# Kernel tuning notes

Measured on AMD Instinct MI355X. Metric: run time of the kernel, lower is better.

The kernel has to match this reference:

```python
import jax, jax.numpy as jnp
import numpy as np

N = 100000      # nodes
E = 3200000     # edges
F_IN = 128      # input node features
G = 64          # graphs in batch
A = 32          # action_shape


def _fanin_uniform(key, shape):
    v = 1.0 / np.sqrt(shape[0])
    return jax.random.uniform(key, shape, jnp.float32, -v, v)


def setup_inputs() -> dict:
    key = jax.random.key(0)
    ks = jax.random.split(key, 16)
    x = jax.random.normal(ks[0], (N, F_IN), jnp.float32)
    edge_index = jax.random.randint(ks[1], (2, E), 0, N, jnp.int64)
    batch = jnp.sort(jax.random.randint(ks[2], (N,), 0, G, jnp.int64))
    init_w = 0.003
    return {
        "x": x,
        "edge_index": edge_index,
        "batch": batch,
        # GCN weights are [in, out] (old-style PyG GCNConv .weight)
        "W1": _fanin_uniform(ks[3], (F_IN, 16)), "b1": jnp.zeros((16,), jnp.float32),
        "W2": _fanin_uniform(ks[4], (16, 64)),   "b2": jnp.zeros((64,), jnp.float32),
        "W3": _fanin_uniform(ks[5], (64, 32)),   "b3": jnp.zeros((32,), jnp.float32),
        # MLP head (Linear stores [out, in]; we keep [in, out] and matmul directly)
        "Wa": _fanin_uniform(ks[6], (32, 64)),   "ba": jnp.zeros((64,), jnp.float32),
        "Wo": jax.random.uniform(ks[7], (64, A), jnp.float32, -init_w, init_w),
        "bo": jnp.zeros((A,), jnp.float32),
    }


def _gcn_conv(x, W, b, src, dst, dinv):
    # GCNConv: D^{-1/2}(A+I)D^{-1/2} X W + b, symmetric norm with self-loops.
    h = x @ W                                   # [N, out] small GEMM
    coef = dinv[src] * dinv[dst]                # [E]
    msg = h[src] * coef[:, None]                # gather + scale (memory-bound)
    agg = jax.ops.segment_sum(msg, dst, num_segments=N)  # scatter-add
    agg = agg + h * (dinv * dinv)[:, None]      # self-loop contribution
    return agg + b


def reference(x, edge_index, batch, W1, b1, W2, b2, W3, b3, Wa, ba, Wo, bo):
    src, dst = edge_index[0], edge_index[1]
    # degree with self-loops (edge weights = 1)
    deg = jax.ops.segment_sum(jnp.ones((E,), x.dtype), dst, num_segments=N) + 1.0
    dinv = jax.lax.rsqrt(deg)

    h = jax.nn.relu(_gcn_conv(x, W1, b1, src, dst, dinv))   # dropout: eval no-op
    h = jax.nn.relu(_gcn_conv(h, W2, b2, src, dst, dinv))
    h = _gcn_conv(h, W3, b3, src, dst, dinv)                # [N, 32]

    # global_mean_pool over batch ids
    sums = jax.ops.segment_sum(h, batch, num_segments=G)            # [G, 32]
    cnts = jax.ops.segment_sum(jnp.ones((N,), h.dtype), batch, num_segments=G)
    pooled = sums / jnp.maximum(cnts, 1.0)[:, None]

    a = jax.nn.relu(pooled @ Wa + ba)
    return jnp.tanh(a @ Wo + bo)                             # [G, A]
```

## Files before the change

kernel.cpp:

```cpp
#include <hip/hip_runtime.h>
#include <hip/hip_bf16.h>
#include <math.h>


#define THREADS 256
#define TCSR 512
#define BSH 8
#define MAXNB 512
#define CH_E 2048
#define CPT 8

__device__ inline unsigned short f2bf(float f) {
    unsigned int u = __float_as_uint(f);
    return (unsigned short)((u + 0x7fffu + ((u >> 16) & 1u)) >> 16);
}
__device__ inline unsigned int pk2bf(float a, float b) {
    return (unsigned int)f2bf(a) | ((unsigned int)f2bf(b) << 16);
}
__device__ inline float bflo(unsigned int u) { return __uint_as_float(u << 16); }
__device__ inline float bfhi(unsigned int u) { return __uint_as_float(u & 0xffff0000u); }
__device__ inline void unpk8(const uint4 u, float* f) {
    f[0] = bflo(u.x); f[1] = bfhi(u.x); f[2] = bflo(u.y); f[3] = bfhi(u.y);
    f[4] = bflo(u.z); f[5] = bfhi(u.z); f[6] = bflo(u.w); f[7] = bfhi(u.w);
}

__global__ void k_countA(const int* __restrict__ dst, unsigned short* __restrict__ lp16,
                         int* __restrict__ cnt_mat, int E, int NB, int NCH) {
    __shared__ int hist[MAXNB];
    int t = threadIdx.x, chunk = blockIdx.x;
    for (int h = t; h < NB; h += THREADS) hist[h] = 0;
    __syncthreads();
    int e0 = chunk * CH_E, e1 = min(E, e0 + CH_E);
    for (int e = e0 + t; e < e1; e += THREADS) {
        int h = dst[e] >> BSH;
        int lp = atomicAdd(&hist[h], 1);
        lp16[e] = (unsigned short)lp;
    }
    __syncthreads();
    for (int h = t; h < NB; h += THREADS) cnt_mat[(size_t)h * NCH + chunk] = hist[h];
}

__global__ void k_sumK1(const int* __restrict__ cnt_mat, int* __restrict__ bucket_tot, int NCH) {
    __shared__ int red[THREADS];
    int b = blockIdx.x, t = threadIdx.x;
    int s = 0;
    for (int c = t; c < NCH; c += THREADS) s += cnt_mat[(size_t)b * NCH + c];
    red[t] = s;
    __syncthreads();
    for (int off = THREADS / 2; off > 0; off >>= 1) {
        if (t < off) red[t] += red[t + off];
        __syncthreads();
    }
    if (t == 0) bucket_tot[b] = red[0];
}

__global__ void k_scanK2(const int* __restrict__ bucket_tot, int* __restrict__ bucket_base,
                         int* __restrict__ rowptr, int NB, int E, int N) {
    __shared__ int sh[MAXNB];
    int t = threadIdx.x;
    int v = (t < NB) ? bucket_tot[t] : 0;
    sh[t] = v;
    __syncthreads();
    for (int off = 1; off < MAXNB; off <<= 1) {
        int u = (t >= off) ? sh[t - off] : 0;
        __syncthreads();
        sh[t] += u;
        __syncthreads();
    }
    if (t < NB) bucket_base[t] = sh[t] - v;
    if (t == 0) { bucket_base[NB] = E; rowptr[N] = E; }
}

__global__ void k_scanK3(const int* __restrict__ cnt_mat, const int* __restrict__ bucket_base,
                         int* __restrict__ offs_mat, int NCH) {
    __shared__ int sh[THREADS];
    int b = blockIdx.x, t = threadIdx.x;
    int c0 = t * CPT;
    int v[CPT];
    int s = 0;
#pragma unroll
    for (int k = 0; k < CPT; ++k) {
        int c = c0 + k;
        v[k] = (c < NCH) ? cnt_mat[(size_t)b * NCH + c] : 0;
        s += v[k];
    }
    sh[t] = s;
    __syncthreads();
    for (int off = 1; off < THREADS; off <<= 1) {
        int u = (t >= off) ? sh[t - off] : 0;
        __syncthreads();
        sh[t] += u;
        __syncthreads();
    }
    int run = bucket_base[b] + sh[t] - s;
#pragma unroll
    for (int k = 0; k < CPT; ++k) {
        int c = c0 + k;
        if (c < NCH) { offs_mat[(size_t)b * NCH + c] = run; run += v[k]; }
    }
}

__global__ void k_scatter2(const int* __restrict__ src, const int* __restrict__ dst,
                           const unsigned short* __restrict__ lp16,
                           const int* __restrict__ offs_mat,
                           unsigned int* __restrict__ bedges, int E, int NB, int NCH) {
    __shared__ int offs[MAXNB];
    int t = threadIdx.x, chunk = blockIdx.x;
    for (int h = t; h < NB; h += THREADS) offs[h] = offs_mat[(size_t)h * NCH + chunk];
    __syncthreads();
    int e0 = chunk * CH_E, e1 = min(E, e0 + CH_E);
    for (int e = e0 + t; e < e1; e += THREADS) {
        int d = dst[e];
        int h = d >> BSH;
        int pos = offs[h] + (int)lp16[e];
        bedges[pos] = ((unsigned int)src[e] << BSH) | (unsigned int)(d & ((1 << BSH) - 1));
    }
}

__global__ void k_bucket_csr(const unsigned int* __restrict__ bedges,
                             const int* __restrict__ bucket_base,
                             int* __restrict__ rowptr, float* __restrict__ dinv,
                             int* __restrict__ csr_src, int N) {
    __shared__ int hist[256];
    __shared__ int sc[256];
    __shared__ int cur[256];
    int t = threadIdx.x;
    int b = blockIdx.x;
    int base = bucket_base[b];
    int end = bucket_base[b + 1];
    if (t < 256) hist[t] = 0;
    __syncthreads();
    for (int i = base + t; i < end; i += TCSR)
        atomicAdd(&hist[bedges[i] & 255], 1);
    __syncthreads();
    int c = 0;
    if (t < 256) { c = hist[t]; sc[t] = c; }
    __syncthreads();
    for (int off = 1; off < 256; off <<= 1) {
        int u = (t >= off && t < 256) ? sc[t - off] : 0;
        __syncthreads();
        if (t < 256) sc[t] += u;
        __syncthreads();
    }
    if (t < 256) {
        int excl = sc[t] - c;
        int node = (b << BSH) + t;
        if (node < N) {
            rowptr[node] = base + excl;
            dinv[node] = (float)(1.0 / sqrt((double)(c + 1)));
        }
        cur[t] = excl;
    }
    __syncthreads();
    for (int i = base + t; i < end; i += TCSR) {
        unsigned int u = bedges[i];
        int ln = (int)(u & 255);
        int p = atomicAdd(&cur[ln], 1);
        csr_src[base + p] = (int)(u >> BSH);
    }
}

__global__ __launch_bounds__(256) void k_gemm1(const float* __restrict__ X,
                        const float* __restrict__ W,
                        const float* __restrict__ dinv, unsigned short* __restrict__ H, int N) {
    __shared__ float Wt[16 * 128];
    int t = threadIdx.x;
    for (int i = t; i < 16 * 128; i += THREADS) {
        int j = i >> 7, k = i & 127;
        Wt[i] = W[k * 16 + j];
    }
    __syncthreads();
    int row = blockIdx.x * THREADS + t;
    if (row >= N) return;
    const float4* xr = (const float4*)(X + (size_t)row * 128);
    float acc[16];
#pragma unroll
    for (int j = 0; j < 16; ++j) acc[j] = 0.0f;
#pragma unroll 4
    for (int k4 = 0; k4 < 32; ++k4) {
        float4 xv = xr[k4];
#pragma unroll
        for (int j = 0; j < 16; ++j) {
            const float4 wv = *(const float4*)&Wt[j * 128 + k4 * 4];
            acc[j] += xv.x * wv.x + xv.y * wv.y + xv.z * wv.z + xv.w * wv.w;
        }
    }
    float di = dinv[row];
    uint4 oa, ob;
    oa.x = pk2bf(acc[0] * di, acc[1] * di);
    oa.y = pk2bf(acc[2] * di, acc[3] * di);
    oa.z = pk2bf(acc[4] * di, acc[5] * di);
    oa.w = pk2bf(acc[6] * di, acc[7] * di);
    ob.x = pk2bf(acc[8] * di, acc[9] * di);
    ob.y = pk2bf(acc[10] * di, acc[11] * di);
    ob.z = pk2bf(acc[12] * di, acc[13] * di);
    ob.w = pk2bf(acc[14] * di, acc[15] * di);
    uint4* outr = (uint4*)(H + (size_t)row * 16);
    outr[0] = oa;
    outr[1] = ob;
}

template<int F, int MODE, int S>
__global__ __launch_bounds__(256) void k_pull(
        const int* __restrict__ rowptr, const int* __restrict__ csr_src,
        const float* __restrict__ dinv, const unsigned short* __restrict__ Hb,
        const float* __restrict__ bias, void* __restrict__ outp,
        const int* __restrict__ batch, float* __restrict__ gsums,
        int N, int G) {
    const int LPN = F / 8;
    const int GRP = LPN * S;
    const int NPB = THREADS / GRP;
    int t = threadIdx.x;
    int idx = t % GRP;
    int fl = idx % LPN;
    int s  = idx / LPN;
    int fo = fl * 8;
    int node = blockIdx.x * NPB + t / GRP;

    float acc[8] = {0.f, 0.f, 0.f, 0.f, 0.f, 0.f, 0.f, 0.f};
    if (node < N) {
        int beg = rowptr[node], end = rowptr[node + 1];
        int i = beg + s;
        for (; i + 3 * S < end; i += 4 * S) {
            int s0 = csr_src[i];
            int s1 = csr_src[i + S];
            int s2 = csr_src[i + 2 * S];
            int s3 = csr_src[i + 3 * S];
            uint4 g0 = *(const uint4*)(Hb + (size_t)s0 * F + fo);
            uint4 g1 = *(const uint4*)(Hb + (size_t)s1 * F + fo);
            uint4 g2 = *(const uint4*)(Hb + (size_t)s2 * F + fo);
            uint4 g3 = *(const uint4*)(Hb + (size_t)s3 * F + fo);
            float f0[8], f1[8], f2[8], f3[8];
            unpk8(g0, f0); unpk8(g1, f1); unpk8(g2, f2); unpk8(g3, f3);
#pragma unroll
            for (int j = 0; j < 8; ++j) acc[j] += (f0[j] + f1[j]) + (f2[j] + f3[j]);
        }
        for (; i < end; i += S) {
            int sv = csr_src[i];
            uint4 g = *(const uint4*)(Hb + (size_t)sv * F + fo);
            float f[8];
            unpk8(g, f);
#pragma unroll
            for (int j = 0; j < 8; ++j) acc[j] += f[j];
        }
    }
#pragma unroll
    for (int j = 0; j < 8; ++j) {
        if (S >= 2) acc[j] += __shfl_xor(acc[j], LPN);
        if (S >= 4) acc[j] += __shfl_xor(acc[j], 2 * LPN);
    }

    if constexpr (MODE == 3) {
        __shared__ float lsum[4][32];
        __shared__ int g0s;
        for (int z = t; z < 4 * 32; z += THREADS) ((float*)lsum)[z] = 0.0f;
        if (t == 0) g0s = batch[blockIdx.x * NPB];
        __syncthreads();
        int g0 = g0s;
        if (node < N && s == 0) {
            uint4 gs = *(const uint4*)(Hb + (size_t)node * F + fo);
            float sf[8];
            unpk8(gs, sf);
            float di = dinv[node];
            int g = batch[node];
            int r = g - g0;
            if ((unsigned)r < 4u) {
#pragma unroll
                for (int j = 0; j < 8; ++j)
                    atomicAdd(&lsum[r][fo + j], di * (acc[j] + sf[j]));
            } else {
#pragma unroll
                for (int j = 0; j < 8; ++j)
                    atomicAdd(&gsums[(size_t)g * 32 + fo + j], di * (acc[j] + sf[j]));
            }
        }
        __syncthreads();
        if (t < 128) {
            int r = t >> 5, f = t & 31;
            int g = g0 + r;
            float v = lsum[r][f];
            if (g < G && v != 0.0f) atomicAdd(&gsums[(size_t)g * 32 + f], v);
        }
    } else {
        if (node < N && s == 0) {
            uint4 gs = *(const uint4*)(Hb + (size_t)node * F + fo);
            float sf[8];
            unpk8(gs, sf);
            float di = dinv[node];
            float tv[8];
#pragma unroll
            for (int j = 0; j < 8; ++j) tv[j] = di * (acc[j] + sf[j]);
            if constexpr (MODE == 1) {
                float w[8];
#pragma unroll
                for (int j = 0; j < 8; ++j) w[j] = fmaxf(tv[j] + bias[fo + j], 0.0f) * di;
                uint4 st;
                st.x = pk2bf(w[0], w[1]); st.y = pk2bf(w[2], w[3]);
                st.z = pk2bf(w[4], w[5]); st.w = pk2bf(w[6], w[7]);
                *(uint4*)((unsigned short*)outp + (size_t)node * F + fo) = st;
            } else {
                float* of = (float*)outp + (size_t)node * F + fo;
                float4 o0, o1;
                o0.x = tv[0]; o0.y = tv[1]; o0.z = tv[2]; o0.w = tv[3];
                o1.x = tv[4]; o1.y = tv[5]; o1.z = tv[6]; o1.w = tv[7];
                ((float4*)of)[0] = o0; ((float4*)of)[1] = o1;
            }
        }
    }
}

__global__ __launch_bounds__(256) void k_mlp(const float* __restrict__ P2,
                      const float* __restrict__ W2, const float* __restrict__ b2,
                      const float* __restrict__ W3, const float* __restrict__ dinv,
                      unsigned short* __restrict__ Hb3, int N) {
    __shared__ float W2t[64][16];
    __shared__ float W3t[32][64];
    __shared__ float b2s[64];
    int t = threadIdx.x;
    for (int i = t; i < 64 * 16; i += THREADS) W2t[i / 16][i % 16] = W2[(i % 16) * 64 + (i / 16)];
    for (int i = t; i < 32 * 64; i += THREADS) W3t[i / 64][i % 64] = W3[(i % 64) * 32 + (i / 64)];
    if (t < 64) b2s[t] = b2[t];
    __syncthreads();
    int n = blockIdx.x * THREADS + t;
    if (n >= N) return;
    const float4* pr = (const float4*)(P2 + (size_t)n * 16);
    float4 p0 = pr[0], p1 = pr[1], p2v = pr[2], p3 = pr[3];
    float p[16] = { p0.x, p0.y, p0.z, p0.w, p1.x, p1.y, p1.z, p1.w,
                    p2v.x, p2v.y, p2v.z, p2v.w, p3.x, p3.y, p3.z, p3.w };
    float a[64];
#pragma unroll
    for (int j = 0; j < 64; ++j) {
        const float4* w = (const float4*)W2t[j];
        float4 w0 = w[0], w1 = w[1], w2q = w[2], w3q = w[3];
        float acc = b2s[j];
        acc += p[0] * w0.x + p[1] * w0.y + p[2] * w0.z + p[3] * w0.w;
        acc += p[4] * w1.x + p[5] * w1.y + p[6] * w1.z + p[7] * w1.w;
        acc += p[8] * w2q.x + p[9] * w2q.y + p[10] * w2q.z + p[11] * w2q.w;
        acc += p[12] * w3q.x + p[13] * w3q.y + p[14] * w3q.z + p[15] * w3q.w;
        a[j] = fmaxf(acc, 0.0f);
    }
    float di = dinv[n];
    unsigned short* outr = Hb3 + (size_t)n * 32;
#pragma unroll
    for (int m = 0; m < 32; m += 2) {
        float o0 = 0.0f, o1 = 0.0f;
        const float4* wa = (const float4*)W3t[m];
        const float4* wb = (const float4*)W3t[m + 1];
#pragma unroll
        for (int q = 0; q < 16; ++q) {
            float4 va = wa[q], vb = wb[q];
            o0 += a[4 * q] * va.x + a[4 * q + 1] * va.y + a[4 * q + 2] * va.z + a[4 * q + 3] * va.w;
            o1 += a[4 * q] * vb.x + a[4 * q + 1] * vb.y + a[4 * q + 2] * vb.z + a[4 * q + 3] * vb.w;
        }
        *(unsigned int*)(outr + m) = pk2bf(o0 * di, o1 * di);
    }
}

__global__ void k_zero_f(float* p, int n) {
    int i = blockIdx.x * blockDim.x + threadIdx.x;
    if (i < n) p[i] = 0.0f;
}

__global__ void k_head(const float* __restrict__ sums, const int* __restrict__ batch, int N,
                       const float* __restrict__ b3,
                       const float* __restrict__ Wa, const float* __restrict__ ba,
                       const float* __restrict__ Wo, const float* __restrict__ bo,
                       float* __restrict__ out) {
    int g = blockIdx.x;
    int j = threadIdx.x;
    int lo = 0, hi = N;
    while (lo < hi) { int m = (lo + hi) >> 1; if (batch[m] < g) lo = m + 1; else hi = m; }
    int start = lo;
    lo = start; hi = N;
    while (lo < hi) { int m = (lo + hi) >> 1; if (batch[m] < g + 1) lo = m + 1; else hi = m; }
    int cnt = lo - start;
    float inv = 1.0f / (float)(cnt > 0 ? cnt : 1);

    __shared__ float p[32];
    __shared__ float a[64];
    if (j < 32) p[j] = sums[g * 32 + j] * inv + b3[j];
    __syncthreads();
    float acc = ba[j];
#pragma unroll
    for (int k = 0; k < 32; ++k) acc += p[k] * Wa[k * 64 + j];
    a[j] = fmaxf(acc, 0.0f);
    __syncthreads();
    if (j < 32) {
        float acc2 = bo[j];
#pragma unroll
        for (int k = 0; k < 64; ++k) acc2 += a[k] * Wo[k * 32 + j];
        out[g * 32 + j] = tanhf(acc2);
    }
}

static inline int cdiv(long long a, int b) { return (int)((a + b - 1) / b); }
static inline size_t align256(size_t x) { return (x + 255) & ~(size_t)255; }

extern "C" void kernel_launch(void* const* d_in, const int* in_sizes, int n_in,
                              void* d_out, int out_size, void* d_ws, size_t ws_size,
                              hipStream_t stream) {
    const float* x     = (const float*)d_in[0];
    const int*   edge  = (const int*)d_in[1];
    const int*   batch = (const int*)d_in[2];
    const float* W1 = (const float*)d_in[3];  const float* b1 = (const float*)d_in[4];
    const float* W2 = (const float*)d_in[5];  const float* b2 = (const float*)d_in[6];
    const float* W3 = (const float*)d_in[7];  const float* b3 = (const float*)d_in[8];
    const float* Wa = (const float*)d_in[9];  const float* ba = (const float*)d_in[10];
    const float* Wo = (const float*)d_in[11]; const float* bo = (const float*)d_in[12];

    const int E = in_sizes[1] / 2;
    const int N = in_sizes[2];
    const int G = 64;
    const int NB = cdiv(N, 1 << BSH);
    const int NCH = cdiv(E, CH_E);

    const int* srcp = edge;
    const int* dstp = edge + E;

    char* base = (char*)d_ws;
    size_t off = 0;
    float* dinv   = (float*)(base + off); off = align256(off + sizeof(float) * N);
    unsigned short* lp16 = (unsigned short*)(base + off); off = align256(off + sizeof(short) * E);
    int* cnt_mat  = (int*)(base + off); off = align256(off + sizeof(int) * (size_t)NB * NCH);
    int* offs_mat = (int*)(base + off); off = align256(off + sizeof(int) * (size_t)NB * NCH);
    int* btot     = (int*)(base + off); off = align256(off + sizeof(int) * (NB + 1));
    int* bbase    = (int*)(base + off); off = align256(off + sizeof(int) * (NB + 1));
    unsigned int* bedges = (unsigned int*)(base + off); off = align256(off + sizeof(int) * E);
    int* rowptr   = (int*)(base + off); off = align256(off + sizeof(int) * (N + 1));
    int* csr_src  = (int*)(base + off); off = align256(off + sizeof(int) * E);
    unsigned short* Hb1 = (unsigned short*)(base + off); off = align256(off + sizeof(short) * (size_t)N * 16);
    unsigned short* Hb2 = (unsigned short*)(base + off); off = align256(off + sizeof(short) * (size_t)N * 16);
    float* P2     = (float*)(base + off); off = align256(off + sizeof(float) * (size_t)N * 16);
    unsigned short* Hb3 = (unsigned short*)(base + off); off = align256(off + sizeof(short) * (size_t)N * 32);
    float* sums   = (float*)(base + off); off = align256(off + sizeof(float) * G * 32);

    k_countA<<<NCH, THREADS, 0, stream>>>(dstp, lp16, cnt_mat, E, NB, NCH);
    k_sumK1<<<NB, THREADS, 0, stream>>>(cnt_mat, btot, NCH);
    k_scanK2<<<1, MAXNB, 0, stream>>>(btot, bbase, rowptr, NB, E, N);
    k_scanK3<<<NB, THREADS, 0, stream>>>(cnt_mat, bbase, offs_mat, NCH);
    k_scatter2<<<NCH, THREADS, 0, stream>>>(srcp, dstp, lp16, offs_mat, bedges, E, NB, NCH);

    k_bucket_csr<<<NB, TCSR, 0, stream>>>(bedges, bbase, rowptr, dinv, csr_src, N);

    k_gemm1<<<cdiv(N, THREADS), THREADS, 0, stream>>>(x, W1, dinv, Hb1, N);
    k_pull<16, 1, 4><<<cdiv(N, 32), THREADS, 0, stream>>>(rowptr, csr_src, dinv, Hb1, b1, Hb2,
                                                          nullptr, nullptr, N, G);

    k_pull<16, 2, 4><<<cdiv(N, 32), THREADS, 0, stream>>>(rowptr, csr_src, dinv, Hb2, nullptr, P2,
                                                          nullptr, nullptr, N, G);

    k_mlp<<<cdiv(N, THREADS), THREADS, 0, stream>>>(P2, W2, b2, W3, dinv, Hb3, N);

    k_zero_f<<<cdiv(G * 32, THREADS), THREADS, 0, stream>>>(sums, G * 32);
    k_pull<32, 3, 2><<<cdiv(N, 32), THREADS, 0, stream>>>(rowptr, csr_src, dinv, Hb3, nullptr,
                                                          nullptr, batch, sums, N, G);

    k_head<<<G, 64, 0, stream>>>(sums, batch, N, b3, Wa, ba, Wo, bo, (float*)d_out);
}
```

Measured before the change: 339.4 us.

## Split per-node MLP across 8 threads with shared-memory hidden activations

The fused per-node MLP (16->64 relu ->32) used to run one node per thread, holding 64 hidden activations in registers. Now 8 threads cooperate on each pair of nodes: each computes a slice of the hidden layer, stages it in padded shared memory, then computes a slice of the outputs. This cuts register pressure and spreads the work over more threads to raise occupancy and parallelism. In exchange it adds a block barrier, extra shared memory traffic and strided 2-byte output stores instead of packed 4-byte stores.

```diff
diff --git a/kernel.cpp b/kernel.cpp
--- a/kernel.cpp
+++ b/kernel.cpp
@@ -313,46 +313,84 @@
                       const float* __restrict__ W2, const float* __restrict__ b2,
                       const float* __restrict__ W3, const float* __restrict__ dinv,
                       unsigned short* __restrict__ Hb3, int N) {
-    __shared__ float W2t[64][16];
-    __shared__ float W3t[32][64];
+    __shared__ float W2p[64 * 20];
+    __shared__ float W3p[32 * 68];
     __shared__ float b2s[64];
+    __shared__ float a_sh[64 * 72];
     int t = threadIdx.x;
-    for (int i = t; i < 64 * 16; i += THREADS) W2t[i / 16][i % 16] = W2[(i % 16) * 64 + (i / 16)];
-    for (int i = t; i < 32 * 64; i += THREADS) W3t[i / 64][i % 64] = W3[(i % 64) * 32 + (i / 64)];
+    for (int i = t; i < 64 * 16; i += THREADS) {
+        int j = i >> 4, k = i & 15;
+        W2p[j * 20 + k] = W2[k * 64 + j];
+    }
+    for (int i = t; i < 32 * 64; i += THREADS) {
+        int m = i >> 6, k = i & 63;
+        W3p[m * 68 + k] = W3[k * 32 + m];
+    }
     if (t < 64) b2s[t] = b2[t];
     __syncthreads();
-    int n = blockIdx.x * THREADS + t;
-    if (n >= N) return;
-    const float4* pr = (const float4*)(P2 + (size_t)n * 16);
-    float4 p0 = pr[0], p1 = pr[1], p2v = pr[2], p3 = pr[3];
-    float p[16] = { p0.x, p0.y, p0.z, p0.w, p1.x, p1.y, p1.z, p1.w,
-                    p2v.x, p2v.y, p2v.z, p2v.w, p3.x, p3.y, p3.z, p3.w };
-    float a[64];
-#pragma unroll
-    for (int j = 0; j < 64; ++j) {
-        const float4* w = (const float4*)W2t[j];
-        float4 w0 = w[0], w1 = w[1], w2q = w[2], w3q = w[3];
-        float acc = b2s[j];
-        acc += p[0] * w0.x + p[1] * w0.y + p[2] * w0.z + p[3] * w0.w;
-        acc += p[4] * w1.x + p[5] * w1.y + p[6] * w1.z + p[7] * w1.w;
-        acc += p[8] * w2q.x + p[9] * w2q.y + p[10] * w2q.z + p[11] * w2q.w;
-        acc += p[12] * w3q.x + p[13] * w3q.y + p[14] * w3q.z + p[15] * w3q.w;
-        a[j] = fmaxf(acc, 0.0f);
-    }
-    float di = dinv[n];
-    unsigned short* outr = Hb3 + (size_t)n * 32;
-#pragma unroll
-    for (int m = 0; m < 32; m += 2) {
-        float o0 = 0.0f, o1 = 0.0f;
-        const float4* wa = (const float4*)W3t[m];
-        const float4* wb = (const float4*)W3t[m + 1];
-#pragma unroll
-        for (int q = 0; q < 16; ++q) {
-            float4 va = wa[q], vb = wb[q];
-            o0 += a[4 * q] * va.x + a[4 * q + 1] * va.y + a[4 * q + 2] * va.z + a[4 * q + 3] * va.w;
-            o1 += a[4 * q] * vb.x + a[4 * q + 1] * vb.y + a[4 * q + 2] * vb.z + a[4 * q + 3] * vb.w;
-        }
-        *(unsigned int*)(outr + m) = pk2bf(o0 * di, o1 * di);
+
+    int q = t & 7;
+    int gb = t >> 3;
+    int n0 = blockIdx.x * 64 + gb;
+    int n1 = n0 + 32;
+    bool v0 = n0 < N, v1 = n1 < N;
+    int c0 = v0 ? n0 : 0, c1 = v1 ? n1 : 0;
+
+    const float4* pr0 = (const float4*)(P2 + (size_t)c0 * 16);
+    const float4* pr1 = (const float4*)(P2 + (size_t)c1 * 16);
+    float4 x0 = pr0[0], x1 = pr0[1], x2 = pr0[2], x3 = pr0[3];
+    float4 y0 = pr1[0], y1 = pr1[1], y2 = pr1[2], y3 = pr1[3];
+    float p0[16] = { x0.x, x0.y, x0.z, x0.w, x1.x, x1.y, x1.z, x1.w,
+                     x2.x, x2.y, x2.z, x2.w, x3.x, x3.y, x3.z, x3.w };
+    float p1[16] = { y0.x, y0.y, y0.z, y0.w, y1.x, y1.y, y1.z, y1.w,
+                     y2.x, y2.y, y2.z, y2.w, y3.x, y3.y, y3.z, y3.w };
+
+#pragma unroll
+    for (int jj = 0; jj < 8; ++jj) {
+        int j = q + 8 * jj;
+        const float4* w = (const float4*)&W2p[j * 20];
+        float4 w0 = w[0], w1 = w[1], w2 = w[2], w3 = w[3];
+        float bb = b2s[j];
+        float acc0 = bb, acc1 = bb;
+        acc0 += p0[0] * w0.x + p0[1] * w0.y + p0[2] * w0.z + p0[3] * w0.w;
+        acc0 += p0[4] * w1.x + p0[5] * w1.y + p0[6] * w1.z + p0[7] * w1.w;
+        acc0 += p0[8] * w2.x + p0[9] * w2.y + p0[10] * w2.z + p0[11] * w2.w;
+        acc0 += p0[12] * w3.x + p0[13] * w3.y + p0[14] * w3.z + p0[15] * w3.w;
+        acc1 += p1[0] * w0.x + p1[1] * w0.y + p1[2] * w0.z + p1[3] * w0.w;
+        acc1 += p1[4] * w1.x + p1[5] * w1.y + p1[6] * w1.z + p1[7] * w1.w;
+        acc1 += p1[8] * w2.x + p1[9] * w2.y + p1[10] * w2.z + p1[11] * w2.w;
+        acc1 += p1[12] * w3.x + p1[13] * w3.y + p1[14] * w3.z + p1[15] * w3.w;
+        a_sh[gb * 72 + j] = fmaxf(acc0, 0.0f);
+        a_sh[(gb + 32) * 72 + j] = fmaxf(acc1, 0.0f);
+    }
+    __syncthreads();
+
+    float acc[2][4] = {{0.f, 0.f, 0.f, 0.f}, {0.f, 0.f, 0.f, 0.f}};
+    const float* ar0 = &a_sh[gb * 72];
+    const float* ar1 = &a_sh[(gb + 32) * 72];
+#pragma unroll
+    for (int kk = 0; kk < 16; ++kk) {
+        float4 a0 = *(const float4*)(ar0 + 4 * kk);
+        float4 a1 = *(const float4*)(ar1 + 4 * kk);
+#pragma unroll
+        for (int mm = 0; mm < 4; ++mm) {
+            int m = q + 8 * mm;
+            float4 w = *(const float4*)&W3p[m * 68 + 4 * kk];
+            acc[0][mm] += a0.x * w.x + a0.y * w.y + a0.z * w.z + a0.w * w.w;
+            acc[1][mm] += a1.x * w.x + a1.y * w.y + a1.z * w.z + a1.w * w.w;
+        }
+    }
+    if (v0) {
+        float d0 = dinv[c0];
+        unsigned short* o = Hb3 + (size_t)n0 * 32;
+#pragma unroll
+        for (int mm = 0; mm < 4; ++mm) o[q + 8 * mm] = f2bf(acc[0][mm] * d0);
+    }
+    if (v1) {
+        float d1 = dinv[c1];
+        unsigned short* o = Hb3 + (size_t)n1 * 32;
+#pragma unroll
+        for (int mm = 0; mm < 4; ++mm) o[q + 8 * mm] = f2bf(acc[1][mm] * d1);
     }
 }
 
@@ -449,7 +487,7 @@
     k_pull<16, 2, 4><<<cdiv(N, 32), THREADS, 0, stream>>>(rowptr, csr_src, dinv, Hb2, nullptr, P2,
                                                           nullptr, nullptr, N, G);
 
-    k_mlp<<<cdiv(N, THREADS), THREADS, 0, stream>>>(P2, W2, b2, W3, dinv, Hb3, N);
+    k_mlp<<<cdiv(N, 64), THREADS, 0, stream>>>(P2, W2, b2, W3, dinv, Hb3, N);
 
     k_zero_f<<<cdiv(G * 32, THREADS), THREADS, 0, stream>>>(sums, G * 32);
     k_pull<32, 3, 2><<<cdiv(N, 32), THREADS, 0, stream>>>(rowptr, csr_src, dinv, Hb3, nullptr,
```

Result: slower. 347.7 us (+2.4%).

## Compute k_mlp per-node 16→64→32 MLP with bf16 MFMA instructions

Applied to the files above, without the earlier changes.

Rewrites the per-node MLP kernel (aggregated layer-2 input times W2, bias and ReLU, then times W3 and scaled by dinv) to use 16x16x32 bf16 MFMA instructions. Each wavefront now handles 16 nodes instead of each thread handling one node with scalar FMAs. The intermediate activations are staged through LDS in bf16 to form the second MFMA operand. Inputs, weights and the hidden layer are now rounded to bf16, which adds precision loss. Each thread also loads weights straight from global memory without coalescing.

```diff
diff --git a/kernel.cpp b/kernel.cpp
--- a/kernel.cpp
+++ b/kernel.cpp
@@ -9,6 +9,9 @@
 #define MAXNB 512
 #define CH_E 2048
 #define CPT 8
+
+typedef __attribute__((ext_vector_type(8))) short short8;
+typedef __attribute__((ext_vector_type(4))) float f32x4;
 
 __device__ inline unsigned short f2bf(float f) {
     unsigned int u = __float_as_uint(f);
@@ -313,46 +316,101 @@
                       const float* __restrict__ W2, const float* __restrict__ b2,
                       const float* __restrict__ W3, const float* __restrict__ dinv,
                       unsigned short* __restrict__ Hb3, int N) {
-    __shared__ float W2t[64][16];
-    __shared__ float W3t[32][64];
-    __shared__ float b2s[64];
+    __shared__ unsigned int aTd[4][32][17];
     int t = threadIdx.x;
-    for (int i = t; i < 64 * 16; i += THREADS) W2t[i / 16][i % 16] = W2[(i % 16) * 64 + (i / 16)];
-    for (int i = t; i < 32 * 64; i += THREADS) W3t[i / 64][i % 64] = W3[(i % 64) * 32 + (i / 64)];
-    if (t < 64) b2s[t] = b2[t];
-    __syncthreads();
-    int n = blockIdx.x * THREADS + t;
-    if (n >= N) return;
-    const float4* pr = (const float4*)(P2 + (size_t)n * 16);
-    float4 p0 = pr[0], p1 = pr[1], p2v = pr[2], p3 = pr[3];
-    float p[16] = { p0.x, p0.y, p0.z, p0.w, p1.x, p1.y, p1.z, p1.w,
-                    p2v.x, p2v.y, p2v.z, p2v.w, p3.x, p3.y, p3.z, p3.w };
-    float a[64];
-#pragma unroll
-    for (int j = 0; j < 64; ++j) {
-        const float4* w = (const float4*)W2t[j];
-        float4 w0 = w[0], w1 = w[1], w2q = w[2], w3q = w[3];
-        float acc = b2s[j];
-        acc += p[0] * w0.x + p[1] * w0.y + p[2] * w0.z + p[3] * w0.w;
-        acc += p[4] * w1.x + p[5] * w1.y + p[6] * w1.z + p[7] * w1.w;
-        acc += p[8] * w2q.x + p[9] * w2q.y + p[10] * w2q.z + p[11] * w2q.w;
-        acc += p[12] * w3q.x + p[13] * w3q.y + p[14] * w3q.z + p[15] * w3q.w;
-        a[j] = fmaxf(acc, 0.0f);
-    }
-    float di = dinv[n];
-    unsigned short* outr = Hb3 + (size_t)n * 32;
-#pragma unroll
-    for (int m = 0; m < 32; m += 2) {
-        float o0 = 0.0f, o1 = 0.0f;
-        const float4* wa = (const float4*)W3t[m];
-        const float4* wb = (const float4*)W3t[m + 1];
-#pragma unroll
-        for (int q = 0; q < 16; ++q) {
-            float4 va = wa[q], vb = wb[q];
-            o0 += a[4 * q] * va.x + a[4 * q + 1] * va.y + a[4 * q + 2] * va.z + a[4 * q + 3] * va.w;
-            o1 += a[4 * q] * vb.x + a[4 * q + 1] * vb.y + a[4 * q + 2] * vb.z + a[4 * q + 3] * vb.w;
-        }
-        *(unsigned int*)(outr + m) = pk2bf(o0 * di, o1 * di);
+    int w = t >> 6;
+    int l = t & 63;
+    int g = l >> 4;
+    int c = l & 15;
+    int node = blockIdx.x * 64 + w * 16 + c;
+    bool nv = node < N;
+    int cn = nv ? node : 0;
+
+    short8 w2f[4];
+#pragma unroll
+    for (int mi = 0; mi < 4; ++mi) {
+        short8 f = {0, 0, 0, 0, 0, 0, 0, 0};
+        if (g < 2) {
+            int j = 16 * mi + c;
+#pragma unroll
+            for (int e = 0; e < 8; ++e)
+                f[e] = (short)f2bf(W2[(8 * g + e) * 64 + j]);
+        }
+        w2f[mi] = f;
+    }
+    short8 w3f[2][2];
+#pragma unroll
+    for (int mt = 0; mt < 2; ++mt)
+#pragma unroll
+        for (int kt = 0; kt < 2; ++kt) {
+            short8 f;
+#pragma unroll
+            for (int e = 0; e < 8; ++e)
+                f[e] = (short)f2bf(W3[(32 * kt + 8 * g + e) * 32 + 16 * mt + c]);
+            w3f[mt][kt] = f;
+        }
+    float b2v[16];
+#pragma unroll
+    for (int mi = 0; mi < 4; ++mi)
+#pragma unroll
+        for (int r = 0; r < 4; ++r)
+            b2v[4 * mi + r] = b2[16 * mi + 4 * g + r];
+
+    short8 pf = {0, 0, 0, 0, 0, 0, 0, 0};
+    if (g < 2) {
+        const float4* pr = (const float4*)(P2 + (size_t)cn * 16 + 8 * g);
+        float4 p0 = pr[0], p1 = pr[1];
+        pf[0] = (short)f2bf(p0.x); pf[1] = (short)f2bf(p0.y);
+        pf[2] = (short)f2bf(p0.z); pf[3] = (short)f2bf(p0.w);
+        pf[4] = (short)f2bf(p1.x); pf[5] = (short)f2bf(p1.y);
+        pf[6] = (short)f2bf(p1.z); pf[7] = (short)f2bf(p1.w);
+    }
+
+    f32x4 zero = {0.f, 0.f, 0.f, 0.f};
+    f32x4 acc1[4];
+#pragma unroll
+    for (int mi = 0; mi < 4; ++mi)
+        acc1[mi] = __builtin_amdgcn_mfma_f32_16x16x32_bf16(w2f[mi], pf, zero, 0, 0, 0);
+
+#pragma unroll
+    for (int mi = 0; mi < 4; ++mi) {
+        float a0 = fmaxf(acc1[mi][0] + b2v[4 * mi + 0], 0.f);
+        float a1 = fmaxf(acc1[mi][1] + b2v[4 * mi + 1], 0.f);
+        float a2 = fmaxf(acc1[mi][2] + b2v[4 * mi + 2], 0.f);
+        float a3 = fmaxf(acc1[mi][3] + b2v[4 * mi + 3], 0.f);
+        aTd[w][8 * mi + 2 * g][c]     = pk2bf(a0, a1);
+        aTd[w][8 * mi + 2 * g + 1][c] = pk2bf(a2, a3);
+    }
+    __syncthreads();
+
+    short8 bfr[2];
+#pragma unroll
+    for (int kt = 0; kt < 2; ++kt) {
+        short8 f;
+#pragma unroll
+        for (int i = 0; i < 4; ++i) {
+            unsigned int d = aTd[w][16 * kt + 4 * g + i][c];
+            f[2 * i]     = (short)(d & 0xffffu);
+            f[2 * i + 1] = (short)(d >> 16);
+        }
+        bfr[kt] = f;
+    }
+
+    f32x4 acc2[2] = {{0.f, 0.f, 0.f, 0.f}, {0.f, 0.f, 0.f, 0.f}};
+#pragma unroll
+    for (int mt = 0; mt < 2; ++mt)
+#pragma unroll
+        for (int kt = 0; kt < 2; ++kt)
+            acc2[mt] = __builtin_amdgcn_mfma_f32_16x16x32_bf16(w3f[mt][kt], bfr[kt], acc2[mt], 0, 0, 0);
+
+    if (nv) {
+        float di = dinv[node];
+        unsigned short* o = Hb3 + (size_t)node * 32;
+#pragma unroll
+        for (int mt = 0; mt < 2; ++mt) {
+            *(unsigned int*)(o + 16 * mt + 4 * g)     = pk2bf(acc2[mt][0] * di, acc2[mt][1] * di);
+            *(unsigned int*)(o + 16 * mt + 4 * g + 2) = pk2bf(acc2[mt][2] * di, acc2[mt][3] * di);
+        }
     }
 }
 
@@ -449,7 +507,7 @@
     k_pull<16, 2, 4><<<cdiv(N, 32), THREADS, 0, stream>>>(rowptr, csr_src, dinv, Hb2, nullptr, P2,
                                                           nullptr, nullptr, N, G);
 
-    k_mlp<<<cdiv(N, THREADS), THREADS, 0, stream>>>(P2, W2, b2, W3, dinv, Hb3, N);
+    k_mlp<<<cdiv(N, 64), THREADS, 0, stream>>>(P2, W2, b2, W3, dinv, Hb3, N);
 
     k_zero_f<<<cdiv(G * 32, THREADS), THREADS, 0, stream>>>(sums, G * 32);
     k_pull<32, 3, 2><<<cdiv(N, 32), THREADS, 0, stream>>>(rowptr, csr_src, dinv, Hb3, nullptr,
```

Result: faster. 310.5 us (-8.5%).
